# Kernel tuning notes

Hardware: AMD Instinct MI355X
Metric: run time of the kernel (lower is better)

Reference implementation:

```python
import jax, jax.numpy as jnp
import numpy as np

LIMIT_A = -0.1
LIMIT_B = 1.1
MASK_INIT_MEAN = float(np.log(1 - 0.2) - np.log(0.2))  # droprate_init = 0.2

B, T, I, H = 64, 512, 1024, 1024


def _hard_concrete_gate(mask_logits):
    # deterministic (eval) gate: hardtanh(sigmoid(mask) * (limit_b - limit_a) + limit_a, 0, 1)
    return jnp.clip(jax.nn.sigmoid(mask_logits) * (LIMIT_B - LIMIT_A) + LIMIT_A, 0.0, 1.0)


def setup_inputs() -> dict:
    key = jax.random.key(0)
    ks = jax.random.split(key, 9)
    xavier = float(np.sqrt(6.0 / (H + I)))
    seq = jax.random.normal(ks[0], (B, T, I), dtype=jnp.float32)
    w_ih = jax.random.uniform(ks[1], (H, I), jnp.float32, -xavier, xavier)
    w_hh = jax.random.uniform(ks[2], (H, H), jnp.float32, -xavier, xavier)
    b_ih = jnp.zeros((H,), jnp.float32)
    b_hh = jnp.zeros((H,), jnp.float32)
    # mask logits ~ N(log((1-droprate)/droprate), 0.01)
    w_ih_mask = MASK_INIT_MEAN + 0.01 * jax.random.normal(ks[3], (H, I), jnp.float32)
    w_hh_mask = MASK_INIT_MEAN + 0.01 * jax.random.normal(ks[4], (H, H), jnp.float32)
    b_ih_mask = MASK_INIT_MEAN + 0.01 * jax.random.normal(ks[5], (H,), jnp.float32)
    b_hh_mask = MASK_INIT_MEAN + 0.01 * jax.random.normal(ks[6], (H,), jnp.float32)
    return {
        "seq": seq,
        "w_ih": w_ih, "w_ih_mask": w_ih_mask,
        "w_hh": w_hh, "w_hh_mask": w_hh_mask,
        "b_ih": b_ih, "b_ih_mask": b_ih_mask,
        "b_hh": b_hh, "b_hh_mask": b_hh_mask,
    }


def reference(seq, w_ih, w_ih_mask, w_hh, w_hh_mask, b_ih, b_ih_mask, b_hh, b_hh_mask):
    # gated (L0 hard-concrete, deterministic) weights
    W_ih = _hard_concrete_gate(w_ih_mask) * w_ih  # [H, I]
    W_hh = _hard_concrete_gate(w_hh_mask) * w_hh  # [H, H]
    B_ih = _hard_concrete_gate(b_ih_mask) * b_ih  # [H]
    B_hh = _hard_concrete_gate(b_hh_mask) * b_hh  # [H]

    # precompute input projection for all timesteps: [B, T, H]
    x_proj = jnp.einsum('bti,hi->bth', seq, W_ih) + B_ih + B_hh

    h0 = jnp.zeros((seq.shape[0], W_hh.shape[0]), seq.dtype)

    def step(h, xp_t):  # xp_t: [B, H]
        h_new = jnp.tanh(xp_t + h @ W_hh.T)
        return h_new, h_new

    h_last, hs = jax.lax.scan(step, h0, jnp.swapaxes(x_proj, 0, 1))  # hs: [T, B, H]
    output = jnp.swapaxes(hs, 0, 1)  # [B, T, H] (batch_first)
    return output, h_last[None]  # hidden: [num_layers*num_dirs, B, H]
```

## Files before the change

kernel.cpp:

```cpp
#include <hip/hip_runtime.h>
#include <cmath>


typedef _Float16 v8h __attribute__((ext_vector_type(8)));
typedef float    v4f __attribute__((ext_vector_type(4)));
typedef unsigned long long u64;
typedef unsigned int u32;

#define BB 64
#define TT 512
#define HH 1024
#define OUT_MAIN (BB * TT * HH)
#define OFF_WIH  0u
#define OFF_WHH  (2u << 20)
#define OFF_BIAS (4u << 20)
#define OFF_HBUF ((4u << 20) + 8192u)
#define OFF_SEQF ((4u << 20) + 8192u + 262144u)
#define OFF_CNT  ((4u << 20) + 8192u + 262144u + 1024u)

#define ALD(p)    __hip_atomic_load((p),        __ATOMIC_RELAXED, __HIP_MEMORY_SCOPE_AGENT)
#define AST(p, v) __hip_atomic_store((p), (v),  __ATOMIC_RELAXED, __HIP_MEMORY_SCOPE_AGENT)

__device__ __forceinline__ float hc_gate(float x) {
    float s = 1.0f / (1.0f + __expf(-x));
    float g = s * 1.2f - 0.1f;
    return fminf(1.0f, fmaxf(0.0f, g));
}

__device__ __forceinline__ float fast_tanh(float x) {
    float e = __expf(2.0f * x);
    return 1.0f - 2.0f * __builtin_amdgcn_rcpf(e + 1.0f);
}

__global__ void prep_kernel(const float* __restrict__ w_ih, const float* __restrict__ w_ih_mask,
                            const float* __restrict__ w_hh, const float* __restrict__ w_hh_mask,
                            const float* __restrict__ b_ih, const float* __restrict__ b_ih_mask,
                            const float* __restrict__ b_hh, const float* __restrict__ b_hh_mask,
                            _Float16* __restrict__ Wih, _Float16* __restrict__ Whh,
                            float* __restrict__ bias, _Float16* __restrict__ hbuf,
                            int* __restrict__ seqf, int* __restrict__ cnt) {
    const int idx = blockIdx.x * 256 + threadIdx.x;
    Wih[idx] = (_Float16)(hc_gate(w_ih_mask[idx]) * w_ih[idx]);
    Whh[idx] = (_Float16)(hc_gate(w_hh_mask[idx]) * w_hh[idx]);
    if (idx < HH)
        bias[idx] = hc_gate(b_ih_mask[idx]) * b_ih[idx] + hc_gate(b_hh_mask[idx]) * b_hh[idx];
    if (idx < 131072) hbuf[idx] = (_Float16)0.0f;
    if (idx < 256) seqf[idx] = 0;
    if (idx < 128) cnt[idx] = 0;
}

__global__ __launch_bounds__(256, 1) void fused_kernel(
        const float* __restrict__ seq, const _Float16* __restrict__ Wih,
        const _Float16* __restrict__ Whh, const float* __restrict__ bias,
        float* __restrict__ out, _Float16* __restrict__ hbuf,
        int* __restrict__ seqf, int* __restrict__ cnt) {
    __shared__ __align__(16) char smem[38912];

    const int tid  = threadIdx.x;
    const int lane = tid & 63;
    const int w    = tid >> 6;

    if (blockIdx.x >= 32) {
        _Float16 (*As)[40] = (_Float16 (*)[40])smem;
        _Float16 (*Bs)[40] = (_Float16 (*)[40])(smem + 10240);

        const int gbid   = blockIdx.x - 32;
        const int trange = gbid >> 9;
        const int rem    = gbid & 511;
        const int bb     = rem >> 3;
        const int njw    = rem & 7;
        const int m0 = bb * 512 + trange * 128;
        const int n0 = njw * 128;
        const int mw = (w >> 1) * 64, nw = (w & 1) * 64;

        const int sr = tid >> 1;
        const int sc = (tid & 1) * 16;

        const float*    aSrc = seq + (m0 + sr) * HH + sc;
        const _Float16* bSrc = Wih + (n0 + sr) * HH + sc;

        const v4f vzero = {0.f, 0.f, 0.f, 0.f};
        v4f acc[4][4];
#pragma unroll
        for (int i = 0; i < 4; i++)
#pragma unroll
            for (int j = 0; j < 4; j++) acc[i][j] = vzero;

        const int arow = mw + (lane & 15);
        const int brow = nw + (lane & 15);
        const int kq   = (lane >> 4) * 8;

        for (int k0 = 0; k0 < HH; k0 += 32) {
            float4 f0 = *(const float4*)(aSrc + 0);
            float4 f1 = *(const float4*)(aSrc + 4);
            float4 f2 = *(const float4*)(aSrc + 8);
            float4 f3 = *(const float4*)(aSrc + 12);
            v8h a0 = {(_Float16)f0.x, (_Float16)f0.y, (_Float16)f0.z, (_Float16)f0.w,
                      (_Float16)f1.x, (_Float16)f1.y, (_Float16)f1.z, (_Float16)f1.w};
            v8h a1 = {(_Float16)f2.x, (_Float16)f2.y, (_Float16)f2.z, (_Float16)f2.w,
                      (_Float16)f3.x, (_Float16)f3.y, (_Float16)f3.z, (_Float16)f3.w};
            v8h b0 = *(const v8h*)(bSrc + 0);
            v8h b1 = *(const v8h*)(bSrc + 8);
            *(v8h*)&As[sr][sc]     = a0;
            *(v8h*)&As[sr][sc + 8] = a1;
            *(v8h*)&Bs[sr][sc]     = b0;
            *(v8h*)&Bs[sr][sc + 8] = b1;
            __syncthreads();

            v8h af[4], bf[4];
#pragma unroll
            for (int mi = 0; mi < 4; mi++) af[mi] = *(const v8h*)&As[mi * 16 + arow][kq];
#pragma unroll
            for (int ni = 0; ni < 4; ni++) bf[ni] = *(const v8h*)&Bs[ni * 16 + brow][kq];
#pragma unroll
            for (int mi = 0; mi < 4; mi++)
#pragma unroll
                for (int ni = 0; ni < 4; ni++)
                    acc[mi][ni] = __builtin_amdgcn_mfma_f32_16x16x32_f16(af[mi], bf[ni], acc[mi][ni], 0, 0, 0);
            __syncthreads();
            aSrc += 32;
            bSrc += 32;
        }

        const int colb = lane & 15;
        const int rowq = (lane >> 4) * 4;
#pragma unroll
        for (int ni = 0; ni < 4; ni++) {
            const int col = n0 + nw + ni * 16 + colb;
            const float bz = bias[col];
#pragma unroll
            for (int mi = 0; mi < 4; mi++) {
                const int row = m0 + mw + mi * 16 + rowq;
#pragma unroll
                for (int r = 0; r < 4; r++) {
                    union { float f; u32 u; } cv;
                    cv.f = acc[mi][ni][r] + bz;
                    AST((u32*)&out[(row + r) * HH + col], cv.u);
                }
            }
        }
        __syncthreads();
        if (tid == 0)
            __hip_atomic_fetch_add(&cnt[trange * 32 + (bb >> 4) * 8 + njw], 1,
                                   __ATOMIC_RELAXED, __HIP_MEMORY_SCOPE_AGENT);
        return;
    }

    u64*      hlds  = (u64*)smem;
    _Float16* tbase = (_Float16*)(smem + 32768);

    const int bid = blockIdx.x;
    const int g   = bid >> 3;
    const int jw  = bid & 7;

    const int l15 = lane & 15;
    const int kq  = (lane >> 4) * 8;
    const int bq  = (lane >> 4) * 4;

    const int col0 = jw * 128 + w * 32 + l15;

    v8h Wf[64];
    {
        const _Float16* w0 = Whh + col0 * 1024 + kq;
        const _Float16* w1 = Whh + (col0 + 16) * 1024 + kq;
#pragma unroll
        for (int c = 0; c < 32; c++) {
            Wf[c * 2 + 0] = *(const v8h*)(w0 + c * 32);
            Wf[c * 2 + 1] = *(const v8h*)(w1 + c * 32);
        }
    }

    {
        u64* q = &hlds[(jw * 4 + w) * 128 + lane * 2];
        q[0] = 0ull; q[1] = 0ull;
    }

    {
        const int* c0 = &cnt[0 * 32 + g * 8 + jw];
        while (ALD(c0) < 16) __builtin_amdgcn_s_sleep(8);
        asm volatile("" ::: "memory");
    }
    float xp[2][4];
#pragma unroll
    for (int r = 0; r < 4; r++) {
        const u32* xs = (const u32*)(out + ((g * 16 + bq + r) * TT + 0) * HH + col0);
        union { u32 u; float f; } v0, v1;
        v0.u = ALD(xs); v1.u = ALD(xs + 16);
        xp[0][r] = v0.f; xp[1][r] = v1.f;
    }

    const int pollIdx = (lane < 8 && lane != jw) ? (lane * 4 + w) : -1;
    _Float16* tw = tbase + w * 640;

    for (int t = 0; t < TT; t++) {
        int* sqp = seqf + ((t & 1) * 4 + g) * 32;
        for (;;) {
            int ok = 1;
            if (pollIdx >= 0) ok = (ALD(sqp + pollIdx) >= t) ? 1 : 0;
            if (__all(ok)) break;
            __builtin_amdgcn_s_sleep(1);
        }
        asm volatile("" ::: "memory");

        {
            const u64* hbp = (const u64*)(hbuf + ((t & 1) * 4 + g) * 16384);
            u64 dv[16];
#pragma unroll
            for (int i = 0; i < 8; i++) {
                if (i != jw) {
                    const u64* p = hbp + (i * 4 + w) * 128 + lane * 2;
                    dv[2 * i]     = ALD(p);
                    dv[2 * i + 1] = ALD(p + 1);
                }
            }
#pragma unroll
            for (int i = 0; i < 8; i++) {
                if (i != jw) {
                    u64* q = &hlds[(i * 4 + w) * 128 + lane * 2];
                    q[0] = dv[2 * i];
                    q[1] = dv[2 * i + 1];
                }
            }
        }
        __syncthreads();

        v4f aA0 = {0.f, 0.f, 0.f, 0.f}, aA1 = aA0, aB0 = aA0, aB1 = aA0;
#pragma unroll
        for (int cc = 0; cc < 8; cc++) {
            const u64* q = &hlds[cc * 512 + lane * 2];
            v8h h0 = *(const v8h*)(q);
            v8h h1 = *(const v8h*)(q + 128);
            v8h h2 = *(const v8h*)(q + 256);
            v8h h3 = *(const v8h*)(q + 384);
            aA0 = __builtin_amdgcn_mfma_f32_16x16x32_f16(h0, Wf[(cc * 4 + 0) * 2 + 0], aA0, 0, 0, 0);
            aA1 = __builtin_amdgcn_mfma_f32_16x16x32_f16(h0, Wf[(cc * 4 + 0) * 2 + 1], aA1, 0, 0, 0);
            aB0 = __builtin_amdgcn_mfma_f32_16x16x32_f16(h1, Wf[(cc * 4 + 1) * 2 + 0], aB0, 0, 0, 0);
            aB1 = __builtin_amdgcn_mfma_f32_16x16x32_f16(h1, Wf[(cc * 4 + 1) * 2 + 1], aB1, 0, 0, 0);
            aA0 = __builtin_amdgcn_mfma_f32_16x16x32_f16(h2, Wf[(cc * 4 + 2) * 2 + 0], aA0, 0, 0, 0);
            aA1 = __builtin_amdgcn_mfma_f32_16x16x32_f16(h2, Wf[(cc * 4 + 2) * 2 + 1], aA1, 0, 0, 0);
            aB0 = __builtin_amdgcn_mfma_f32_16x16x32_f16(h3, Wf[(cc * 4 + 3) * 2 + 0], aB0, 0, 0, 0);
            aB1 = __builtin_amdgcn_mfma_f32_16x16x32_f16(h3, Wf[(cc * 4 + 3) * 2 + 1], aB1, 0, 0, 0);
        }
        const v4f av0 = aA0 + aB0;
        const v4f av1 = aA1 + aB1;

        float hv[2][4];
#pragma unroll
        for (int r = 0; r < 4; r++) {
            hv[0][r] = fast_tanh(xp[0][r] + av0[r]);
            hv[1][r] = fast_tanh(xp[1][r] + av1[r]);
            const int row = bq + r;
            tw[row * 40 + l15]      = (_Float16)hv[0][r];
            tw[row * 40 + 16 + l15] = (_Float16)hv[1][r];
        }
        union { v8h v; u64 u[2]; } U;
        U.v = *(const v8h*)(tw + (lane & 15) * 40 + (lane >> 4) * 8);

        if (t + 1 < TT) {
            u64* dst = (u64*)(hbuf + (((t + 1) & 1) * 4 + g) * 16384) + (jw * 4 + w) * 128 + lane * 2;
            AST(dst,     U.u[0]);
            AST(dst + 1, U.u[1]);
            asm volatile("s_waitcnt vmcnt(0)" ::: "memory");
            if (lane == 0)
                AST(seqf + (((t + 1) & 1) * 4 + g) * 32 + jw * 4 + w, t + 1);
        }
        __syncthreads();

        {
            u64* q = &hlds[(jw * 4 + w) * 128 + lane * 2];
            q[0] = U.u[0];
            q[1] = U.u[1];
        }

#pragma unroll
        for (int r = 0; r < 4; r++) {
            const int bg = g * 16 + bq + r;
            float* o = out + (bg * TT + t) * HH + col0;
            o[0]  = hv[0][r];
            o[16] = hv[1][r];
            if (t == TT - 1) {
                float* o2 = out + OUT_MAIN + bg * HH + col0;
                o2[0]  = hv[0][r];
                o2[16] = hv[1][r];
            }
        }
        if (t + 1 < TT) {
            if (((t + 1) & 127) == 0) {
                const int* cc = &cnt[((t + 1) >> 7) * 32 + g * 8 + jw];
                while (ALD(cc) < 16) __builtin_amdgcn_s_sleep(8);
                asm volatile("" ::: "memory");
            }
#pragma unroll
            for (int r = 0; r < 4; r++) {
                const u32* xs = (const u32*)(out + ((g * 16 + bq + r) * TT + (t + 1)) * HH + col0);
                union { u32 u; float f; } v0, v1;
                v0.u = ALD(xs); v1.u = ALD(xs + 16);
                xp[0][r] = v0.f; xp[1][r] = v1.f;
            }
        }
    }
}

extern "C" void kernel_launch(void* const* d_in, const int* in_sizes, int n_in,
                              void* d_out, int out_size, void* d_ws, size_t ws_size,
                              hipStream_t stream) {
    const float* seq       = (const float*)d_in[0];
    const float* w_ih      = (const float*)d_in[1];
    const float* w_ih_mask = (const float*)d_in[2];
    const float* w_hh      = (const float*)d_in[3];
    const float* w_hh_mask = (const float*)d_in[4];
    const float* b_ih      = (const float*)d_in[5];
    const float* b_ih_mask = (const float*)d_in[6];
    const float* b_hh      = (const float*)d_in[7];
    const float* b_hh_mask = (const float*)d_in[8];

    float* out = (float*)d_out;
    char*  ws  = (char*)d_ws;
    _Float16* Wih  = (_Float16*)(ws + OFF_WIH);
    _Float16* Whh  = (_Float16*)(ws + OFF_WHH);
    float*    bias = (float*)(ws + OFF_BIAS);
    _Float16* hbuf = (_Float16*)(ws + OFF_HBUF);
    int*      seqf = (int*)(ws + OFF_SEQF);
    int*      cnt  = (int*)(ws + OFF_CNT);

    prep_kernel<<<dim3(4096), dim3(256), 0, stream>>>(w_ih, w_ih_mask, w_hh, w_hh_mask,
                                                      b_ih, b_ih_mask, b_hh, b_hh_mask,
                                                      Wih, Whh, bias, hbuf, seqf, cnt);
    fused_kernel<<<dim3(2080), dim3(256), 0, stream>>>(seq, Wih, Whh, bias, out,
                                                       hbuf, seqf, cnt);
}
```

Baseline: 2.175 ms.

## Overlap recurrent MFMA on wave-owned hidden slices with the block barrier

The recurrent loop is templated on the wave index so each wave computes its own K-slices (its previous h kept in registers and the remote slices just loaded from global) before the __syncthreads. Only the slices produced by other waves are read back from LDS after the barrier. This shortens the critical path after the barrier and removes the separate LDS write of the wave's own slice at the end of the step. It also raises wave priority with s_setprio. The cost is an extra load of one weight fragment pair, higher register pressure, and four template instantiations that grow the code.

```diff
diff --git a/kernel.cpp b/kernel.cpp
--- a/kernel.cpp
+++ b/kernel.cpp
@@ -47,6 +47,176 @@
     if (idx < 131072) hbuf[idx] = (_Float16)0.0f;
     if (idx < 256) seqf[idx] = 0;
     if (idx < 128) cnt[idx] = 0;
+}
+
+template<int W>
+__device__ __forceinline__ void rnn_loop(
+        int g, int jw, int lane,
+        const _Float16* __restrict__ Whh, float* __restrict__ out,
+        _Float16* __restrict__ hbuf, int* __restrict__ seqf,
+        int* __restrict__ cnt, u64* hlds, _Float16* tbase) {
+
+    const int l15 = lane & 15;
+    const int kq  = (lane >> 4) * 8;
+    const int bq  = (lane >> 4) * 4;
+    const int col0 = jw * 128 + W * 32 + l15;
+
+    v8h Wf[64];
+    {
+        const _Float16* w0 = Whh + col0 * 1024 + kq;
+        const _Float16* w1 = Whh + (col0 + 16) * 1024 + kq;
+#pragma unroll
+        for (int c = 0; c < 32; c++) {
+            Wf[c * 2 + 0] = *(const v8h*)(w0 + c * 32);
+            Wf[c * 2 + 1] = *(const v8h*)(w1 + c * 32);
+        }
+    }
+    v8h WfOwn0, WfOwn1;
+    {
+        const int cown = jw * 4 + W;
+        WfOwn0 = *(const v8h*)(Whh + col0 * 1024 + cown * 32 + kq);
+        WfOwn1 = *(const v8h*)(Whh + (col0 + 16) * 1024 + cown * 32 + kq);
+    }
+
+    union HU { v8h v; u64 u[2]; };
+    HU U; U.u[0] = 0ull; U.u[1] = 0ull;
+
+    __builtin_amdgcn_s_setprio(1);
+
+    {
+        const int* c0 = &cnt[g * 8 + jw];
+        while (ALD(c0) < 16) __builtin_amdgcn_s_sleep(8);
+        asm volatile("" ::: "memory");
+    }
+    float xp[2][4];
+#pragma unroll
+    for (int r = 0; r < 4; r++) {
+        const u32* xs = (const u32*)(out + ((g * 16 + bq + r) * TT) * HH + col0);
+        union { u32 u; float f; } v0, v1;
+        v0.u = ALD(xs); v1.u = ALD(xs + 16);
+        xp[0][r] = v0.f; xp[1][r] = v1.f;
+    }
+
+    const int pollIdx = (lane < 8 && lane != jw) ? (lane * 4 + W) : -1;
+    _Float16* tw = tbase + W * 640;
+
+    for (int t = 0; t < TT; t++) {
+        int* sqp = seqf + ((t & 1) * 4 + g) * 32;
+        for (;;) {
+            int ok = 1;
+            if (pollIdx >= 0) ok = (ALD(sqp + pollIdx) >= t) ? 1 : 0;
+            if (__all(ok)) break;
+            __builtin_amdgcn_s_sleep(1);
+        }
+        asm volatile("" ::: "memory");
+
+        HU dv[8];
+        {
+            const u64* hbp = (const u64*)(hbuf + ((t & 1) * 4 + g) * 16384);
+#pragma unroll
+            for (int i = 0; i < 8; i++) {
+                if (i != jw) {
+                    const u64* p = hbp + (i * 4 + W) * 128 + lane * 2;
+                    dv[i].u[0] = ALD(p);
+                    dv[i].u[1] = ALD(p + 1);
+                }
+            }
+        }
+        {
+            u64* q = &hlds[(jw * 4 + W) * 128 + lane * 2];
+            q[0] = U.u[0]; q[1] = U.u[1];
+#pragma unroll
+            for (int i = 0; i < 8; i++) {
+                if (i != jw) {
+                    u64* qq = &hlds[(i * 4 + W) * 128 + lane * 2];
+                    qq[0] = dv[i].u[0]; qq[1] = dv[i].u[1];
+                }
+            }
+        }
+        v4f rA = {0.f, 0.f, 0.f, 0.f}, rB = rA;
+        rA = __builtin_amdgcn_mfma_f32_16x16x32_f16(U.v, WfOwn0, rA, 0, 0, 0);
+        rB = __builtin_amdgcn_mfma_f32_16x16x32_f16(U.v, WfOwn1, rB, 0, 0, 0);
+#pragma unroll
+        for (int i = 0; i < 8; i++) {
+            if (i != jw) {
+                rA = __builtin_amdgcn_mfma_f32_16x16x32_f16(dv[i].v, Wf[(i * 4 + W) * 2 + 0], rA, 0, 0, 0);
+                rB = __builtin_amdgcn_mfma_f32_16x16x32_f16(dv[i].v, Wf[(i * 4 + W) * 2 + 1], rB, 0, 0, 0);
+            }
+        }
+        __syncthreads();
+
+        v4f aA0 = {0.f, 0.f, 0.f, 0.f}, aA1 = aA0, aB0 = aA0, aB1 = aA0;
+#pragma unroll
+        for (int cc = 0; cc < 8; cc++) {
+            const u64* qb = &hlds[cc * 512 + lane * 2];
+#pragma unroll
+            for (int qq = 0; qq < 4; qq++) {
+                if (qq == W) continue;
+                v8h h = *(const v8h*)(qb + qq * 128);
+                if (qq & 1) {
+                    aB0 = __builtin_amdgcn_mfma_f32_16x16x32_f16(h, Wf[(cc * 4 + qq) * 2 + 0], aB0, 0, 0, 0);
+                    aB1 = __builtin_amdgcn_mfma_f32_16x16x32_f16(h, Wf[(cc * 4 + qq) * 2 + 1], aB1, 0, 0, 0);
+                } else {
+                    aA0 = __builtin_amdgcn_mfma_f32_16x16x32_f16(h, Wf[(cc * 4 + qq) * 2 + 0], aA0, 0, 0, 0);
+                    aA1 = __builtin_amdgcn_mfma_f32_16x16x32_f16(h, Wf[(cc * 4 + qq) * 2 + 1], aA1, 0, 0, 0);
+                }
+            }
+        }
+        const v4f av0 = (aA0 + aB0) + rA;
+        const v4f av1 = (aA1 + aB1) + rB;
+
+        float hv[2][4];
+#pragma unroll
+        for (int r = 0; r < 4; r++) {
+            hv[0][r] = fast_tanh(xp[0][r] + av0[r]);
+            hv[1][r] = fast_tanh(xp[1][r] + av1[r]);
+            const int row = bq + r;
+            tw[row * 40 + l15]      = (_Float16)hv[0][r];
+            tw[row * 40 + 16 + l15] = (_Float16)hv[1][r];
+        }
+        {
+            HU Un;
+            Un.v = *(const v8h*)(tw + (lane & 15) * 40 + (lane >> 4) * 8);
+            U = Un;
+        }
+
+        if (t + 1 < TT) {
+            u64* dst = (u64*)(hbuf + (((t + 1) & 1) * 4 + g) * 16384) + (jw * 4 + W) * 128 + lane * 2;
+            AST(dst,     U.u[0]);
+            AST(dst + 1, U.u[1]);
+            asm volatile("s_waitcnt vmcnt(0)" ::: "memory");
+            if (lane == 0)
+                AST(seqf + (((t + 1) & 1) * 4 + g) * 32 + jw * 4 + W, t + 1);
+        }
+        __syncthreads();
+
+#pragma unroll
+        for (int r = 0; r < 4; r++) {
+            const int bg = g * 16 + bq + r;
+            float* o = out + (bg * TT + t) * HH + col0;
+            o[0]  = hv[0][r];
+            o[16] = hv[1][r];
+            if (t == TT - 1) {
+                float* o2 = out + OUT_MAIN + bg * HH + col0;
+                o2[0]  = hv[0][r];
+                o2[16] = hv[1][r];
+            }
+        }
+        if (t + 1 < TT) {
+            if (((t + 1) & 127) == 0) {
+                const int* cc2 = &cnt[((t + 1) >> 7) * 32 + g * 8 + jw];
+                while (ALD(cc2) < 16) __builtin_amdgcn_s_sleep(8);
+                asm volatile("" ::: "memory");
+            }
+#pragma unroll
+            for (int r = 0; r < 4; r++) {
+                const u32* xs = (const u32*)(out + ((g * 16 + bq + r) * TT + (t + 1)) * HH + col0);
+                union { u32 u; float f; } v0, v1;
+                v0.u = ALD(xs); v1.u = ALD(xs + 16);
+                xp[0][r] = v0.f; xp[1][r] = v1.f;
+            }
+        }
+    }
 }
 
 __global__ __launch_bounds__(256, 1) void fused_kernel(
@@ -149,155 +319,14 @@
     u64*      hlds  = (u64*)smem;
     _Float16* tbase = (_Float16*)(smem + 32768);
 
-    const int bid = blockIdx.x;
-    const int g   = bid >> 3;
-    const int jw  = bid & 7;
-
-    const int l15 = lane & 15;
-    const int kq  = (lane >> 4) * 8;
-    const int bq  = (lane >> 4) * 4;
-
-    const int col0 = jw * 128 + w * 32 + l15;
-
-    v8h Wf[64];
-    {
-        const _Float16* w0 = Whh + col0 * 1024 + kq;
-        const _Float16* w1 = Whh + (col0 + 16) * 1024 + kq;
-#pragma unroll
-        for (int c = 0; c < 32; c++) {
-            Wf[c * 2 + 0] = *(const v8h*)(w0 + c * 32);
-            Wf[c * 2 + 1] = *(const v8h*)(w1 + c * 32);
-        }
-    }
-
-    {
-        u64* q = &hlds[(jw * 4 + w) * 128 + lane * 2];
-        q[0] = 0ull; q[1] = 0ull;
-    }
-
-    {
-        const int* c0 = &cnt[0 * 32 + g * 8 + jw];
-        while (ALD(c0) < 16) __builtin_amdgcn_s_sleep(8);
-        asm volatile("" ::: "memory");
-    }
-    float xp[2][4];
-#pragma unroll
-    for (int r = 0; r < 4; r++) {
-        const u32* xs = (const u32*)(out + ((g * 16 + bq + r) * TT + 0) * HH + col0);
-        union { u32 u; float f; } v0, v1;
-        v0.u = ALD(xs); v1.u = ALD(xs + 16);
-        xp[0][r] = v0.f; xp[1][r] = v1.f;
-    }
-
-    const int pollIdx = (lane < 8 && lane != jw) ? (lane * 4 + w) : -1;
-    _Float16* tw = tbase + w * 640;
-
-    for (int t = 0; t < TT; t++) {
-        int* sqp = seqf + ((t & 1) * 4 + g) * 32;
-        for (;;) {
-            int ok = 1;
-            if (pollIdx >= 0) ok = (ALD(sqp + pollIdx) >= t) ? 1 : 0;
-            if (__all(ok)) break;
-            __builtin_amdgcn_s_sleep(1);
-        }
-        asm volatile("" ::: "memory");
-
-        {
-            const u64* hbp = (const u64*)(hbuf + ((t & 1) * 4 + g) * 16384);
-            u64 dv[16];
-#pragma unroll
-            for (int i = 0; i < 8; i++) {
-                if (i != jw) {
-                    const u64* p = hbp + (i * 4 + w) * 128 + lane * 2;
-                    dv[2 * i]     = ALD(p);
-                    dv[2 * i + 1] = ALD(p + 1);
-                }
-            }
-#pragma unroll
-            for (int i = 0; i < 8; i++) {
-                if (i != jw) {
-                    u64* q = &hlds[(i * 4 + w) * 128 + lane * 2];
-                    q[0] = dv[2 * i];
-                    q[1] = dv[2 * i + 1];
-                }
-            }
-        }
-        __syncthreads();
-
-        v4f aA0 = {0.f, 0.f, 0.f, 0.f}, aA1 = aA0, aB0 = aA0, aB1 = aA0;
-#pragma unroll
-        for (int cc = 0; cc < 8; cc++) {
-            const u64* q = &hlds[cc * 512 + lane * 2];
-            v8h h0 = *(const v8h*)(q);
-            v8h h1 = *(const v8h*)(q + 128);
-            v8h h2 = *(const v8h*)(q + 256);
-            v8h h3 = *(const v8h*)(q + 384);
-            aA0 = __builtin_amdgcn_mfma_f32_16x16x32_f16(h0, Wf[(cc * 4 + 0) * 2 + 0], aA0, 0, 0, 0);
-            aA1 = __builtin_amdgcn_mfma_f32_16x16x32_f16(h0, Wf[(cc * 4 + 0) * 2 + 1], aA1, 0, 0, 0);
-            aB0 = __builtin_amdgcn_mfma_f32_16x16x32_f16(h1, Wf[(cc * 4 + 1) * 2 + 0], aB0, 0, 0, 0);
-            aB1 = __builtin_amdgcn_mfma_f32_16x16x32_f16(h1, Wf[(cc * 4 + 1) * 2 + 1], aB1, 0, 0, 0);
-            aA0 = __builtin_amdgcn_mfma_f32_16x16x32_f16(h2, Wf[(cc * 4 + 2) * 2 + 0], aA0, 0, 0, 0);
-            aA1 = __builtin_amdgcn_mfma_f32_16x16x32_f16(h2, Wf[(cc * 4 + 2) * 2 + 1], aA1, 0, 0, 0);
-            aB0 = __builtin_amdgcn_mfma_f32_16x16x32_f16(h3, Wf[(cc * 4 + 3) * 2 + 0], aB0, 0, 0, 0);
-            aB1 = __builtin_amdgcn_mfma_f32_16x16x32_f16(h3, Wf[(cc * 4 + 3) * 2 + 1], aB1, 0, 0, 0);
-        }
-        const v4f av0 = aA0 + aB0;
-        const v4f av1 = aA1 + aB1;
-
-        float hv[2][4];
-#pragma unroll
-        for (int r = 0; r < 4; r++) {
-            hv[0][r] = fast_tanh(xp[0][r] + av0[r]);
-            hv[1][r] = fast_tanh(xp[1][r] + av1[r]);
-            const int row = bq + r;
-            tw[row * 40 + l15]      = (_Float16)hv[0][r];
-            tw[row * 40 + 16 + l15] = (_Float16)hv[1][r];
-        }
-        union { v8h v; u64 u[2]; } U;
-        U.v = *(const v8h*)(tw + (lane & 15) * 40 + (lane >> 4) * 8);
-
-        if (t + 1 < TT) {
-            u64* dst = (u64*)(hbuf + (((t + 1) & 1) * 4 + g) * 16384) + (jw * 4 + w) * 128 + lane * 2;
-            AST(dst,     U.u[0]);
-            AST(dst + 1, U.u[1]);
-            asm volatile("s_waitcnt vmcnt(0)" ::: "memory");
-            if (lane == 0)
-                AST(seqf + (((t + 1) & 1) * 4 + g) * 32 + jw * 4 + w, t + 1);
-        }
-        __syncthreads();
-
-        {
-            u64* q = &hlds[(jw * 4 + w) * 128 + lane * 2];
-            q[0] = U.u[0];
-            q[1] = U.u[1];
-        }
-
-#pragma unroll
-        for (int r = 0; r < 4; r++) {
-            const int bg = g * 16 + bq + r;
-            float* o = out + (bg * TT + t) * HH + col0;
-            o[0]  = hv[0][r];
-            o[16] = hv[1][r];
-            if (t == TT - 1) {
-                float* o2 = out + OUT_MAIN + bg * HH + col0;
-                o2[0]  = hv[0][r];
-                o2[16] = hv[1][r];
-            }
-        }
-        if (t + 1 < TT) {
-            if (((t + 1) & 127) == 0) {
-                const int* cc = &cnt[((t + 1) >> 7) * 32 + g * 8 + jw];
-                while (ALD(cc) < 16) __builtin_amdgcn_s_sleep(8);
-                asm volatile("" ::: "memory");
-            }
-#pragma unroll
-            for (int r = 0; r < 4; r++) {
-                const u32* xs = (const u32*)(out + ((g * 16 + bq + r) * TT + (t + 1)) * HH + col0);
-                union { u32 u; float f; } v0, v1;
-                v0.u = ALD(xs); v1.u = ALD(xs + 16);
-                xp[0][r] = v0.f; xp[1][r] = v1.f;
-            }
-        }
+    const int g  = blockIdx.x >> 3;
+    const int jw = blockIdx.x & 7;
+
+    switch (w) {
+        case 0: rnn_loop<0>(g, jw, lane, Whh, out, hbuf, seqf, cnt, hlds, tbase); break;
+        case 1: rnn_loop<1>(g, jw, lane, Whh, out, hbuf, seqf, cnt, hlds, tbase); break;
+        case 2: rnn_loop<2>(g, jw, lane, Whh, out, hbuf, seqf, cnt, hlds, tbase); break;
+        default: rnn_loop<3>(g, jw, lane, Whh, out, hbuf, seqf, cnt, hlds, tbase); break;
     }
 }
 
```

Measured after the change: 2.285 ms. 1.05x slower.

## Halve recurrent blocks, each alternating two batch groups per timestep

Applied to the files above, without the earlier changes.

The recurrent part now uses 16 persistent blocks instead of 32. Each block keeps its W_hh slice in registers and interleaves two batch groups (g0, g1) per timestep, so the wait for one group's peer flags overlaps with compute on the other. Each block now also writes its own previous h slice into LDS at the start of every phase. This halves the number of register-resident W_hh copies and frees 16 CUs for the input-projection GEMM. The cost is twice as much serial work per block per timestep. The per-step critical path may get longer if the cross-block synchronisation latency was not the dominant cost.

```diff
diff --git a/kernel.cpp b/kernel.cpp
--- a/kernel.cpp
+++ b/kernel.cpp
@@ -54,17 +54,17 @@
         const _Float16* __restrict__ Whh, const float* __restrict__ bias,
         float* __restrict__ out, _Float16* __restrict__ hbuf,
         int* __restrict__ seqf, int* __restrict__ cnt) {
-    __shared__ __align__(16) char smem[38912];
+    __shared__ __align__(16) char smem[37888];
 
     const int tid  = threadIdx.x;
     const int lane = tid & 63;
     const int w    = tid >> 6;
 
-    if (blockIdx.x >= 32) {
+    if (blockIdx.x >= 16) {
         _Float16 (*As)[40] = (_Float16 (*)[40])smem;
         _Float16 (*Bs)[40] = (_Float16 (*)[40])(smem + 10240);
 
-        const int gbid   = blockIdx.x - 32;
+        const int gbid   = blockIdx.x - 16;
         const int trange = gbid >> 9;
         const int rem    = gbid & 511;
         const int bb     = rem >> 3;
@@ -150,8 +150,9 @@
     _Float16* tbase = (_Float16*)(smem + 32768);
 
     const int bid = blockIdx.x;
-    const int g   = bid >> 3;
     const int jw  = bid & 7;
+    const int g0  = (bid >> 3) * 2;
+    const int g1  = g0 + 1;
 
     const int l15 = lane & 15;
     const int kq  = (lane >> 4) * 8;
@@ -161,38 +162,43 @@
 
     v8h Wf[64];
     {
-        const _Float16* w0 = Whh + col0 * 1024 + kq;
-        const _Float16* w1 = Whh + (col0 + 16) * 1024 + kq;
+        const _Float16* w0p = Whh + col0 * 1024 + kq;
+        const _Float16* w1p = Whh + (col0 + 16) * 1024 + kq;
 #pragma unroll
         for (int c = 0; c < 32; c++) {
-            Wf[c * 2 + 0] = *(const v8h*)(w0 + c * 32);
-            Wf[c * 2 + 1] = *(const v8h*)(w1 + c * 32);
-        }
-    }
+            Wf[c * 2 + 0] = *(const v8h*)(w0p + c * 32);
+            Wf[c * 2 + 1] = *(const v8h*)(w1p + c * 32);
+        }
+    }
+
+    union HU { v8h v; u64 u[2]; };
+    HU U0, U1;
+    U0.u[0] = 0ull; U0.u[1] = 0ull;
+    U1.u[0] = 0ull; U1.u[1] = 0ull;
 
     {
-        u64* q = &hlds[(jw * 4 + w) * 128 + lane * 2];
-        q[0] = 0ull; q[1] = 0ull;
-    }
-
-    {
-        const int* c0 = &cnt[0 * 32 + g * 8 + jw];
+        const int* c0 = &cnt[g0 * 8 + jw];
         while (ALD(c0) < 16) __builtin_amdgcn_s_sleep(8);
+        const int* c1 = &cnt[g1 * 8 + jw];
+        while (ALD(c1) < 16) __builtin_amdgcn_s_sleep(8);
         asm volatile("" ::: "memory");
     }
-    float xp[2][4];
+    float xpA[2][4], xpB[2][4];
 #pragma unroll
     for (int r = 0; r < 4; r++) {
-        const u32* xs = (const u32*)(out + ((g * 16 + bq + r) * TT + 0) * HH + col0);
-        union { u32 u; float f; } v0, v1;
-        v0.u = ALD(xs); v1.u = ALD(xs + 16);
-        xp[0][r] = v0.f; xp[1][r] = v1.f;
+        const u32* xa = (const u32*)(out + ((g0 * 16 + bq + r) * TT + 0) * HH + col0);
+        const u32* xb = (const u32*)(out + ((g1 * 16 + bq + r) * TT + 0) * HH + col0);
+        union { u32 u; float f; } v0, v1, v2, v3;
+        v0.u = ALD(xa); v1.u = ALD(xa + 16);
+        v2.u = ALD(xb); v3.u = ALD(xb + 16);
+        xpA[0][r] = v0.f; xpA[1][r] = v1.f;
+        xpB[0][r] = v2.f; xpB[1][r] = v3.f;
     }
 
     const int pollIdx = (lane < 8 && lane != jw) ? (lane * 4 + w) : -1;
     _Float16* tw = tbase + w * 640;
 
-    for (int t = 0; t < TT; t++) {
+    auto phase = [&](int g, HU& U, float (&xp)[2][4], int t) {
         int* sqp = seqf + ((t & 1) * 4 + g) * 32;
         for (;;) {
             int ok = 1;
@@ -213,6 +219,8 @@
                     dv[2 * i + 1] = ALD(p + 1);
                 }
             }
+            u64* qo = &hlds[(jw * 4 + w) * 128 + lane * 2];
+            qo[0] = U.u[0]; qo[1] = U.u[1];
 #pragma unroll
             for (int i = 0; i < 8; i++) {
                 if (i != jw) {
@@ -253,24 +261,18 @@
             tw[row * 40 + l15]      = (_Float16)hv[0][r];
             tw[row * 40 + 16 + l15] = (_Float16)hv[1][r];
         }
-        union { v8h v; u64 u[2]; } U;
-        U.v = *(const v8h*)(tw + (lane & 15) * 40 + (lane >> 4) * 8);
+        HU Un;
+        Un.v = *(const v8h*)(tw + (lane & 15) * 40 + (lane >> 4) * 8);
 
         if (t + 1 < TT) {
             u64* dst = (u64*)(hbuf + (((t + 1) & 1) * 4 + g) * 16384) + (jw * 4 + w) * 128 + lane * 2;
-            AST(dst,     U.u[0]);
-            AST(dst + 1, U.u[1]);
+            AST(dst,     Un.u[0]);
+            AST(dst + 1, Un.u[1]);
             asm volatile("s_waitcnt vmcnt(0)" ::: "memory");
             if (lane == 0)
                 AST(seqf + (((t + 1) & 1) * 4 + g) * 32 + jw * 4 + w, t + 1);
         }
         __syncthreads();
-
-        {
-            u64* q = &hlds[(jw * 4 + w) * 128 + lane * 2];
-            q[0] = U.u[0];
-            q[1] = U.u[1];
-        }
 
 #pragma unroll
         for (int r = 0; r < 4; r++) {
@@ -298,6 +300,12 @@
                 xp[0][r] = v0.f; xp[1][r] = v1.f;
             }
         }
+        U = Un;
+    };
+
+    for (int t = 0; t < TT; t++) {
+        phase(g0, U0, xpA, t);
+        phase(g1, U1, xpB, t);
     }
 }
 
@@ -326,6 +334,6 @@
     prep_kernel<<<dim3(4096), dim3(256), 0, stream>>>(w_ih, w_ih_mask, w_hh, w_hh_mask,
                                                       b_ih, b_ih_mask, b_hh, b_hh_mask,
                                                       Wih, Whh, bias, hbuf, seqf, cnt);
-    fused_kernel<<<dim3(2080), dim3(256), 0, stream>>>(seq, Wih, Whh, bias, out,
+    fused_kernel<<<dim3(2064), dim3(256), 0, stream>>>(seq, Wih, Whh, bias, out,
                                                        hbuf, seqf, cnt);
 }
```

After: 3.823 ms. 75.8% more time.
